# Performance work log

Hardware: AMD Instinct MI355X
Metric: run time of the kernel (lower is better)

## Reference

```python
import jax, jax.numpy as jnp
import numpy as np

B, T, D, H = 4, 2048, 1024, 16
HD = D // H  # head_dim = 64


def setup_inputs() -> dict:
    key = jax.random.key(0)
    k1, k2, k3 = jax.random.split(key, 3)
    x = jax.random.normal(k1, (B, T, D), dtype=jnp.float32)
    # Linear weights stored [in, out] (transpose of torch's [out, in]); scaled init.
    w_qkv = jax.random.normal(k2, (D, 3 * D), dtype=jnp.float32) / np.sqrt(D)
    b_qkv = jnp.zeros((3 * D,), dtype=jnp.float32)
    w_out = jax.random.normal(k3, (D, D), dtype=jnp.float32) / np.sqrt(D)
    b_out = jnp.zeros((D,), dtype=jnp.float32)
    # Causal mask [1,1,T,T]: 1 where attention allowed (j<=i), 0 elsewhere.
    causal_mask = jnp.tril(jnp.ones((T, T), dtype=jnp.int32))[None, None]
    return {"x": x, "causal_mask": causal_mask, "w_qkv": w_qkv,
            "b_qkv": b_qkv, "w_out": w_out, "b_out": b_out}


def reference(x, causal_mask, w_qkv, b_qkv, w_out, b_out):
    b, t, c = x.shape
    qkv = x @ w_qkv + b_qkv                         # [B,T,3D]
    qkv = qkv.reshape(b, t, 3, H, HD)
    q, k, v = jnp.moveaxis(qkv, 2, 0)               # each [B,T,H,HD]
    q = q.transpose(0, 2, 1, 3)                     # [B,H,T,HD]
    k = k.transpose(0, 2, 1, 3)
    v = v.transpose(0, 2, 1, 3)
    att = jnp.einsum('bhqd,bhkd->bhqk', q, k) / np.sqrt(HD).astype(np.float32)
    att = jnp.where(causal_mask == 0, jnp.float32(-jnp.inf), att)
    att = jax.nn.softmax(att, axis=-1)              # dropout=0.0 (eval)
    y = jnp.einsum('bhqk,bhkd->bhqd', att, v)       # [B,H,T,HD]
    y = y.transpose(0, 2, 1, 3).reshape(b, t, c)    # [B,T,D]
    return y @ w_out + b_out
```

## Files before the change

kernel.cpp:

```cpp
#include <hip/hip_runtime.h>
#include <hip/hip_bf16.h>
#include <stdint.h>

#define BB 4
#define TT 2048
#define DD 1024
#define HH 16
#define HDD 64
#define M1 (BB*TT)
#define N1 (3*DD)
#define KDIM DD

typedef __attribute__((ext_vector_type(8))) short short8;
typedef __attribute__((ext_vector_type(4))) float f32x4;

#if __has_builtin(__builtin_amdgcn_exp2f)
#define EXP2(x) __builtin_amdgcn_exp2f(x)
#else
#define EXP2(x) exp2f(x)
#endif

#define GLOAD_LDS16(gp, lp) \
    __builtin_amdgcn_global_load_lds( \
        (const __attribute__((address_space(1))) void*)(gp), \
        (__attribute__((address_space(3))) void*)(lp), 16, 0, 0)

__device__ __forceinline__ float bf2f(unsigned short u) {
    union { uint32_t u32; float f; } c; c.u32 = ((uint32_t)u) << 16; return c.f;
}
__device__ __forceinline__ unsigned short f2bf(float f) {
    union { float f; uint32_t u32; } c; c.f = f;
    uint32_t u = c.u32;
    return (unsigned short)((u + 0x7FFFu + ((u >> 16) & 1u)) >> 16);
}

template <int CTRL>
__device__ __forceinline__ float dpp_ror(float x) {
    union { float f; int i; } u, r;
    u.f = x;
    r.i = __builtin_amdgcn_update_dpp(u.i, u.i, CTRL, 0xF, 0xF, false);
    return r.f;
}
__device__ __forceinline__ float red_max16(float x) {
    x = fmaxf(x, dpp_ror<0x128>(x));
    x = fmaxf(x, dpp_ror<0x124>(x));
    x = fmaxf(x, dpp_ror<0x122>(x));
    x = fmaxf(x, dpp_ror<0x121>(x));
    return x;
}
__device__ __forceinline__ float red_sum16(float x) {
    x += dpp_ror<0x128>(x);
    x += dpp_ror<0x124>(x);
    x += dpp_ror<0x122>(x);
    x += dpp_ror<0x121>(x);
    return x;
}

__global__ __launch_bounds__(256) void cvt_f32_bf16(
    const float* __restrict__ in, unsigned short* __restrict__ out, int n4)
{
    int i = blockIdx.x * 256 + threadIdx.x;
    if (i >= n4) return;
    float4 v = *(const float4*)&in[(size_t)i * 4];
    ushort4 o;
    o.x = f2bf(v.x); o.y = f2bf(v.y); o.z = f2bf(v.z); o.w = f2bf(v.w);
    *(ushort4*)&out[(size_t)i * 4] = o;
}

__global__ __launch_bounds__(256) void transpose_f32_bf16(
    const float* __restrict__ in, unsigned short* __restrict__ out,
    int R, int C)
{
    __shared__ unsigned short tile[32][33];
    int bx = blockIdx.x;
    int by = blockIdx.y;
    int x = bx*32 + threadIdx.x;
    int y0 = by*32 + threadIdx.y;
    #pragma unroll
    for (int i = 0; i < 32; i += 8)
        tile[threadIdx.y + i][threadIdx.x] = f2bf(in[(size_t)(y0 + i)*C + x]);
    __syncthreads();
    int xo = by*32 + threadIdx.x;
    int yo = bx*32 + threadIdx.y;
    #pragma unroll
    for (int i = 0; i < 32; i += 8)
        out[(size_t)(yo + i)*R + xo] = tile[threadIdx.x][threadIdx.y + i];
}

template <int MODE, int BM, int BN>
__global__ __launch_bounds__(512, 2) void gemm_big(
    const unsigned short* __restrict__ A, const unsigned short* __restrict__ BT,
    const float* __restrict__ bias, void* __restrict__ Cout, void* __restrict__ Cout2,
    int K, int N, int NXT)
{
    constexpr int SHSZ = 2*(BM+BN)*64;
    __shared__ __align__(16) unsigned short Sh[SHSZ];

    const int tid  = threadIdx.x;
    const int lane = tid & 63;
    const int wave = tid >> 6;
    constexpr int WNG = BN/64;
    const int wm = wave / WNG, wn = wave % WNG;
    const int quad = lane >> 4, l16 = lane & 15;

    const int nwg = gridDim.x, cpx = nwg >> 3;
    const int wg = (blockIdx.x & 7)*cpx + (blockIdx.x >> 3);
    const int by = wg / NXT, bx = wg - by*NXT;
    const int m0 = by*BM, n0 = bx*BN;

    f32x4 acc[4][4] = {};
    const int nk = K >> 6;

    auto STAGE = [&](int t, int buf) {
        const int k0 = t << 6;
        unsigned short* Ab = &Sh[buf*(BM*64)];
        unsigned short* Bb = &Sh[2*BM*64 + buf*(BN*64)];
        #pragma unroll
        for (int p = 0; p < BM/64; ++p) {
            int c = p*512 + tid;
            int row = c >> 3, ch = (c & 7) ^ (row & 7);
            GLOAD_LDS16(&A[(size_t)(m0 + row)*K + k0 + ch*8], &Ab[c*8]);
        }
        #pragma unroll
        for (int p = 0; p < BN/64; ++p) {
            int c = p*512 + tid;
            int row = c >> 3, ch = (c & 7) ^ (row & 7);
            GLOAD_LDS16(&BT[(size_t)(n0 + row)*K + k0 + ch*8], &Bb[c*8]);
        }
    };

    STAGE(0, 0);
    STAGE(1, 1);

    for (int t = 0; t < nk; ++t) {
        const int buf = t & 1;
        const unsigned short* Ab = &Sh[buf*(BM*64)];
        const unsigned short* Bb = &Sh[2*BM*64 + buf*(BN*64)];

        if (t == nk - 1) asm volatile("s_waitcnt vmcnt(0)" ::: "memory");
        else             asm volatile("s_waitcnt vmcnt(6)" ::: "memory");
        __builtin_amdgcn_s_barrier();
        __builtin_amdgcn_sched_barrier(0);

        short8 fa[4][2], fb[2][2];

        #pragma unroll
        for (int mi = 0; mi < 4; ++mi)
            #pragma unroll
            for (int kk = 0; kk < 2; ++kk) {
                int row = wm*64 + mi*16 + l16;
                fa[mi][kk] = *(const short8*)&Ab[row*64 + (((kk*4 + quad) ^ (row & 7))*8)];
            }
        #pragma unroll
        for (int ni = 0; ni < 2; ++ni)
            #pragma unroll
            for (int kk = 0; kk < 2; ++kk) {
                int row = wn*64 + ni*16 + l16;
                fb[ni][kk] = *(const short8*)&Bb[row*64 + (((kk*4 + quad) ^ (row & 7))*8)];
            }
        __builtin_amdgcn_s_barrier();
        __builtin_amdgcn_s_setprio(1);
        #pragma unroll
        for (int mi = 0; mi < 4; ++mi)
            #pragma unroll
            for (int ni = 0; ni < 2; ++ni)
                #pragma unroll
                for (int kk = 0; kk < 2; ++kk)
                    acc[mi][ni] = __builtin_amdgcn_mfma_f32_16x16x32_bf16(
                        fa[mi][kk], fb[ni][kk], acc[mi][ni], 0, 0, 0);
        __builtin_amdgcn_s_setprio(0);
        __builtin_amdgcn_s_barrier();

        #pragma unroll
        for (int ni = 0; ni < 2; ++ni)
            #pragma unroll
            for (int kk = 0; kk < 2; ++kk) {
                int row = wn*64 + 32 + ni*16 + l16;
                fb[ni][kk] = *(const short8*)&Bb[row*64 + (((kk*4 + quad) ^ (row & 7))*8)];
            }
        __builtin_amdgcn_s_barrier();
        __builtin_amdgcn_s_setprio(1);
        #pragma unroll
        for (int mi = 0; mi < 4; ++mi)
            #pragma unroll
            for (int ni = 0; ni < 2; ++ni)
                #pragma unroll
                for (int kk = 0; kk < 2; ++kk)
                    acc[mi][2 + ni] = __builtin_amdgcn_mfma_f32_16x16x32_bf16(
                        fa[mi][kk], fb[ni][kk], acc[mi][2 + ni], 0, 0, 0);
        __builtin_amdgcn_s_setprio(0);
        __builtin_amdgcn_s_barrier();

        __builtin_amdgcn_sched_barrier(0);
        if (t + 2 < nk) STAGE(t + 2, buf);
    }

    if (MODE == 2 && n0 >= 2048) {
        constexpr int STR = BM + 8;
        #pragma unroll
        for (int ni = 0; ni < 4; ++ni) {
            int nl = wn*64 + ni*16 + l16;
            float bv = bias[n0 + nl];
            #pragma unroll
            for (int mi = 0; mi < 4; ++mi) {
                ushort4 pk;
                pk.x = f2bf(acc[mi][ni][0] + bv);
                pk.y = f2bf(acc[mi][ni][1] + bv);
                pk.z = f2bf(acc[mi][ni][2] + bv);
                pk.w = f2bf(acc[mi][ni][3] + bv);
                *(ushort4*)&Sh[nl*STR + wm*64 + mi*16 + quad*4] = pk;
            }
        }
        __builtin_amdgcn_s_barrier();
        const int bb = m0 >> 11, t0 = m0 & 2047;
        constexpr int CHROW = BM/8;
        constexpr int NIT = BN*CHROW/512;
        #pragma unroll
        for (int p = 0; p < NIT; ++p) {
            int c = p*512 + tid;
            int row = c / CHROW, ch = c % CHROW;
            int nv = n0 + row - 2048;
            int hv = nv >> 6, dv = nv & 63;
            *(uint4*)&((unsigned short*)Cout2)[((size_t)((bb*16 + hv)*64 + dv))*2048 + t0 + ch*8] =
                *(uint4*)&Sh[row*STR + ch*8];
        }
        return;
    }

    const int cstride = (MODE == 2) ? 2048 : N;
    #pragma unroll
    for (int ni = 0; ni < 4; ++ni) {
        int n = n0 + wn*64 + ni*16 + l16;
        float bv = bias[n];
        #pragma unroll
        for (int mi = 0; mi < 4; ++mi) {
            #pragma unroll
            for (int r = 0; r < 4; ++r) {
                int m = m0 + wm*64 + mi*16 + quad*4 + r;
                float val = acc[mi][ni][r] + bv;
                if (MODE == 1)
                    ((float*)Cout)[(size_t)m*cstride + n] = val;
                else
                    ((unsigned short*)Cout)[(size_t)m*cstride + n] = f2bf(val);
            }
        }
    }
}

#define PST 72
__global__ __launch_bounds__(256, 3) void attn_mfma(
    const unsigned short* __restrict__ QK, const unsigned short* __restrict__ VT,
    unsigned short* __restrict__ Y)
{
    __shared__ __align__(16) unsigned short Sh[16384 + 4*32*PST];

    const int tid  = threadIdx.x;
    const int lane = tid & 63;
    const int wave = tid >> 6;
    const int quad = lane >> 4, l16 = lane & 15;

    const int i = blockIdx.x;
    const int xcd = i & 7, j = i >> 3;
    const int a = j & 7;
    const int u = j >> 3;
    const int bh2 = xcd + 8*u;
    const int b = bh2 >> 4, h = bh2 & 15;
    const size_t qkbase = (size_t)(b*TT) * 2048;
    const size_t vbase  = (size_t)(bh2*64) * 2048;
    const int qcol = h*64, kcol = 1024 + h*64;
    const float C2 = 0.18033688011112042f;

    unsigned short* Pw = &Sh[16384 + wave*(32*PST)];

    const int nk1 = 2*a + 2;
    const int ntot = 34;

    short8 aq[2][2];
    f32x4 o[2][4];
    float mold[2][4], lsum[2][4];
    int q0w = a*128 + wave*32;

    auto LOADQ = [&]() {
        #pragma unroll
        for (int mt = 0; mt < 2; ++mt)
            #pragma unroll
            for (int kk = 0; kk < 2; ++kk)
                aq[mt][kk] = *(const short8*)&QK[qkbase + (size_t)(q0w + mt*16 + l16)*2048
                                                + qcol + kk*32 + quad*8];
        #pragma unroll
        for (int mt = 0; mt < 2; ++mt)
            #pragma unroll
            for (int r = 0; r < 4; ++r) { mold[mt][r] = -3.0e38f; lsum[mt][r] = 0.0f; }
        #pragma unroll
        for (int mt = 0; mt < 2; ++mt)
            #pragma unroll
            for (int dt = 0; dt < 4; ++dt) { f32x4 z = {}; o[mt][dt] = z; }
    };
    auto FINALIZE = [&]() {
        #pragma unroll
        for (int mt = 0; mt < 2; ++mt)
            #pragma unroll
            for (int r = 0; r < 4; ++r) {
                float inv = 1.0f / lsum[mt][r];
                int tq = q0w + mt*16 + quad*4 + r;
                #pragma unroll
                for (int dt = 0; dt < 4; ++dt)
                    Y[((size_t)(b*TT + tq))*DD + h*64 + dt*16 + l16] = f2bf(o[mt][dt][r] * inv);
            }
    };

    auto STAGE = [&](int buf, int k0) {
        unsigned short* Kb = &Sh[buf*4096];
        unsigned short* Vb = &Sh[8192 + buf*4096];
        #pragma unroll
        for (int p = 0; p < 2; ++p) {
            int c = p*256 + tid;
            int r = c >> 3;
            int ch = (c & 7) ^ (r & 7);
            GLOAD_LDS16(&QK[qkbase + (size_t)(k0 + r)*2048 + kcol + ch*8], &Kb[c*8]);
        }
        #pragma unroll
        for (int p = 0; p < 2; ++p) {
            int c = p*256 + tid;
            int r = c >> 3;
            int ch = (c & 7) ^ (r & 7);
            GLOAD_LDS16(&VT[vbase + (size_t)r*2048 + k0 + ch*8], &Vb[c*8]);
        }
    };

    LOADQ();
    STAGE(0, 0);
    asm volatile("s_waitcnt vmcnt(0)" ::: "memory");
    __builtin_amdgcn_s_barrier();

    int cur = 0;
    for (int t = 0; t < ntot; ++t) {
        const int k0 = ((t < nk1) ? t : t - nk1) * 64;
        if (t + 1 < ntot) {
            const int t1 = t + 1;
            STAGE(cur ^ 1, ((t1 < nk1) ? t1 : t1 - nk1) * 64);
        }
        if (t == nk1) {
            FINALIZE();
            q0w = (15 - a)*128 + wave*32;
            LOADQ();
        }

        if (k0 <= q0w + 31) {
            const unsigned short* Kb = &Sh[cur*4096];
            const unsigned short* Vb = &Sh[8192 + cur*4096];

            f32x4 s[2][4];
            #pragma unroll
            for (int nt = 0; nt < 4; ++nt) {
                if (k0 + nt*16 <= q0w + 31) {
                    f32x4 z = {};
                    s[0][nt] = z; s[1][nt] = z;
                    #pragma unroll
                    for (int kk = 0; kk < 2; ++kk) {
                        int r = nt*16 + l16;
                        short8 bk = *(const short8*)&Kb[r*64 + (((kk*4 + quad) ^ (r & 7))*8)];
                        s[0][nt] = __builtin_amdgcn_mfma_f32_16x16x32_bf16(aq[0][kk], bk, s[0][nt], 0, 0, 0);
                        s[1][nt] = __builtin_amdgcn_mfma_f32_16x16x32_bf16(aq[1][kk], bk, s[1][nt], 0, 0, 0);
                    }
                } else {
                    #pragma unroll
                    for (int r = 0; r < 4; ++r) { s[0][nt][r] = -3.0e38f; s[1][nt][r] = -3.0e38f; }
                }
            }

            short8 bv[2][4];
            #pragma unroll
            for (int kk = 0; kk < 2; ++kk)
                #pragma unroll
                for (int dt = 0; dt < 4; ++dt) {
                    int r = dt*16 + l16;
                    bv[kk][dt] = *(const short8*)&Vb[r*64 + (((kk*4 + quad) ^ (r & 7))*8)];
                }

            if (k0 + 63 > q0w) {
                #pragma unroll
                for (int mt = 0; mt < 2; ++mt)
                    #pragma unroll
                    for (int nt = 0; nt < 4; ++nt)
                        #pragma unroll
                        for (int r = 0; r < 4; ++r) {
                            int kg = k0 + nt*16 + l16;
                            int qg = q0w + mt*16 + quad*4 + r;
                            if (kg > qg) s[mt][nt][r] = -3.0e38f;
                        }
            }

            float m2n[2][4], al[2][4];
            #pragma unroll
            for (int mt = 0; mt < 2; ++mt)
                #pragma unroll
                for (int r = 0; r < 4; ++r) {
                    float rm = fmaxf(fmaxf(s[mt][0][r], s[mt][1][r]),
                                     fmaxf(s[mt][2][r], s[mt][3][r]));
                    rm = red_max16(rm);
                    float m2 = fmaxf(mold[mt][r], rm * C2);
                    al[mt][r]  = EXP2(mold[mt][r] - m2);
                    m2n[mt][r] = m2;
                }
            float rs[2][4] = {};
            #pragma unroll
            for (int mt = 0; mt < 2; ++mt)
                #pragma unroll
                for (int nt = 0; nt < 4; ++nt)
                    #pragma unroll
                    for (int r = 0; r < 4; ++r) {
                        float p = EXP2(fmaf(s[mt][nt][r], C2, -m2n[mt][r]));
                        s[mt][nt][r] = p;
                        rs[mt][r] += p;
                    }
            #pragma unroll
            for (int mt = 0; mt < 2; ++mt)
                #pragma unroll
                for (int r = 0; r < 4; ++r) {
                    float tsum = red_sum16(rs[mt][r]);
                    lsum[mt][r] = lsum[mt][r]*al[mt][r] + tsum;
                    mold[mt][r] = m2n[mt][r];
                }

            #pragma unroll
            for (int mt = 0; mt < 2; ++mt)
                #pragma unroll
                for (int nt = 0; nt < 4; ++nt)
                    #pragma unroll
                    for (int r = 0; r < 4; ++r) {
                        union { float f; uint32_t u; } c; c.f = s[mt][nt][r];
                        Pw[(mt*16 + quad*4 + r)*PST + nt*16 + l16] =
                            (unsigned short)((c.u + 0x8000u) >> 16);
                    }

            #pragma unroll
            for (int mt = 0; mt < 2; ++mt)
                #pragma unroll
                for (int dt = 0; dt < 4; ++dt)
                    #pragma unroll
                    for (int r = 0; r < 4; ++r)
                        o[mt][dt][r] *= al[mt][r];
            #pragma unroll
            for (int kk = 0; kk < 2; ++kk) {
                short8 ap0 = *(short8*)&Pw[(     l16)*PST + kk*32 + quad*8];
                short8 ap1 = *(short8*)&Pw[(16 + l16)*PST + kk*32 + quad*8];
                #pragma unroll
                for (int dt = 0; dt < 4; ++dt) {
                    o[0][dt] = __builtin_amdgcn_mfma_f32_16x16x32_bf16(ap0, bv[kk][dt], o[0][dt], 0, 0, 0);
                    o[1][dt] = __builtin_amdgcn_mfma_f32_16x16x32_bf16(ap1, bv[kk][dt], o[1][dt], 0, 0, 0);
                }
            }
        }

        asm volatile("s_waitcnt vmcnt(0)" ::: "memory");
        __builtin_amdgcn_s_barrier();
        cur ^= 1;
    }

    FINALIZE();
}

extern "C" void kernel_launch(void* const* d_in, const int* in_sizes, int n_in,
                              void* d_out, int out_size, void* d_ws, size_t ws_size,
                              hipStream_t stream)
{
    const float* x    = (const float*)d_in[0];
    const float* wqkv = (const float*)d_in[2];
    const float* bqkv = (const float*)d_in[3];
    const float* wout = (const float*)d_in[4];
    const float* bout = (const float*)d_in[5];
    float* out = (float*)d_out;

    char* ws = (char*)d_ws;
    unsigned short* Xb    = (unsigned short*)ws;
    unsigned short* WqkvT = (unsigned short*)(ws + 16777216);
    unsigned short* WoutT = (unsigned short*)(ws + 23068672);
    unsigned short* QK    = (unsigned short*)(ws + 25165824);
    unsigned short* VTb   = (unsigned short*)(ws + 58720256);
    unsigned short* Ybuf  = (unsigned short*)(ws + 75497472);

    cvt_f32_bf16<<<(M1*KDIM/4 + 255)/256, 256, 0, stream>>>(x, Xb, M1*KDIM/4);
    transpose_f32_bf16<<<dim3(N1/32, KDIM/32), dim3(32, 8), 0, stream>>>(wqkv, WqkvT, KDIM, N1);
    transpose_f32_bf16<<<dim3(DD/32, KDIM/32), dim3(32, 8), 0, stream>>>(wout, WoutT, KDIM, DD);
    gemm_big<2, 256, 128><<<dim3(768), 512, 0, stream>>>(Xb, WqkvT, bqkv, QK, VTb, KDIM, N1, 24);
    attn_mfma<<<dim3(512), 256, 0, stream>>>(QK, VTb, Ybuf);
    gemm_big<1, 128, 256><<<dim3(256), 512, 0, stream>>>(Ybuf, WoutT, bout, out, nullptr, KDIM, DD, 4);
}
```

Before: 313.7 us.

## Triple-buffer GEMM LDS and interleave prefetch loads across four MFMA phases

The GEMM main loop moves from two LDS buffers to three rotating buffers. The global-to-LDS prefetch for tile t+2 is split into six parts that are issued between four MFMA sub-phases, instead of in one burst at the end of each iteration. Fragment loads are also regrouped into quadrants so fewer registers are live at once. The aim is to overlap memory traffic with compute and shorten stalls at the loop tail, at the cost of 1.5x the LDS footprint, which may reduce occupancy, and extra barriers per iteration. The vmcnt(6) wait count may no longer match the new per-phase load pattern.

```diff
diff --git a/kernel.cpp b/kernel.cpp
--- a/kernel.cpp
+++ b/kernel.cpp
@@ -93,13 +93,14 @@
     const float* __restrict__ bias, void* __restrict__ Cout, void* __restrict__ Cout2,
     int K, int N, int NXT)
 {
-    constexpr int SHSZ = 2*(BM+BN)*64;
-    __shared__ __align__(16) unsigned short Sh[SHSZ];
+    constexpr int TBUF = (BM + BN) * 64;
+    constexpr int NPART = (BM + BN) / 64;
+    __shared__ __align__(16) unsigned short Sh[3 * TBUF];
 
     const int tid  = threadIdx.x;
     const int lane = tid & 63;
     const int wave = tid >> 6;
-    constexpr int WNG = BN/64;
+    constexpr int WNG = BN / 64;
     const int wm = wave / WNG, wn = wave % WNG;
     const int quad = lane >> 4, l16 = lane & 15;
 
@@ -111,88 +112,124 @@
     f32x4 acc[4][4] = {};
     const int nk = K >> 6;
 
-    auto STAGE = [&](int t, int buf) {
-        const int k0 = t << 6;
-        unsigned short* Ab = &Sh[buf*(BM*64)];
-        unsigned short* Bb = &Sh[2*BM*64 + buf*(BN*64)];
-        #pragma unroll
-        for (int p = 0; p < BM/64; ++p) {
-            int c = p*512 + tid;
+    auto STAGE_PART = [&](int tt, int bufi, int part) {
+        const int k0 = tt << 6;
+        unsigned short* base = &Sh[bufi * TBUF];
+        if ((part + 1) * 512 <= BM * 8) {
+            int c = part*512 + tid;
             int row = c >> 3, ch = (c & 7) ^ (row & 7);
-            GLOAD_LDS16(&A[(size_t)(m0 + row)*K + k0 + ch*8], &Ab[c*8]);
-        }
-        #pragma unroll
-        for (int p = 0; p < BN/64; ++p) {
-            int c = p*512 + tid;
+            GLOAD_LDS16(&A[(size_t)(m0 + row)*K + k0 + ch*8], &base[c*8]);
+        } else {
+            int c = part*512 + tid - BM*8;
             int row = c >> 3, ch = (c & 7) ^ (row & 7);
-            GLOAD_LDS16(&BT[(size_t)(n0 + row)*K + k0 + ch*8], &Bb[c*8]);
+            GLOAD_LDS16(&BT[(size_t)(n0 + row)*K + k0 + ch*8], &base[BM*64 + c*8]);
         }
     };
 
-    STAGE(0, 0);
-    STAGE(1, 1);
-
+    #pragma unroll
+    for (int p = 0; p < NPART; ++p) STAGE_PART(0, 0, p);
+    #pragma unroll
+    for (int p = 0; p < NPART; ++p) STAGE_PART(1, 1, p);
+
+    int bR = 0;
     for (int t = 0; t < nk; ++t) {
-        const int buf = t & 1;
-        const unsigned short* Ab = &Sh[buf*(BM*64)];
-        const unsigned short* Bb = &Sh[2*BM*64 + buf*(BN*64)];
-
-        if (t == nk - 1) asm volatile("s_waitcnt vmcnt(0)" ::: "memory");
+        const unsigned short* Ab = &Sh[bR * TBUF];
+        const unsigned short* Bb = &Sh[bR * TBUF + BM*64];
+        const int bS = (bR + 2 >= 3) ? bR - 1 : bR + 2;
+        const bool pf = (t + 2 < nk);
+
+        if (t >= nk - 1) asm volatile("s_waitcnt vmcnt(0)" ::: "memory");
         else             asm volatile("s_waitcnt vmcnt(6)" ::: "memory");
         __builtin_amdgcn_s_barrier();
         __builtin_amdgcn_sched_barrier(0);
 
-        short8 fa[4][2], fb[2][2];
-
-        #pragma unroll
-        for (int mi = 0; mi < 4; ++mi)
+        short8 fa0[2][2], fa1[2][2], fb0[2][2], fb1[2][2];
+
+        #pragma unroll
+        for (int i = 0; i < 2; ++i)
             #pragma unroll
             for (int kk = 0; kk < 2; ++kk) {
-                int row = wm*64 + mi*16 + l16;
-                fa[mi][kk] = *(const short8*)&Ab[row*64 + (((kk*4 + quad) ^ (row & 7))*8)];
-            }
-        #pragma unroll
-        for (int ni = 0; ni < 2; ++ni)
+                int row = wm*64 + i*16 + l16;
+                fa0[i][kk] = *(const short8*)&Ab[row*64 + (((kk*4 + quad) ^ (row & 7))*8)];
+            }
+        #pragma unroll
+        for (int j = 0; j < 2; ++j)
             #pragma unroll
             for (int kk = 0; kk < 2; ++kk) {
-                int row = wn*64 + ni*16 + l16;
-                fb[ni][kk] = *(const short8*)&Bb[row*64 + (((kk*4 + quad) ^ (row & 7))*8)];
-            }
+                int row = wn*64 + j*16 + l16;
+                fb0[j][kk] = *(const short8*)&Bb[row*64 + (((kk*4 + quad) ^ (row & 7))*8)];
+            }
+        if (pf) { STAGE_PART(t+2, bS, 0); STAGE_PART(t+2, bS, 1); }
         __builtin_amdgcn_s_barrier();
         __builtin_amdgcn_s_setprio(1);
         #pragma unroll
-        for (int mi = 0; mi < 4; ++mi)
-            #pragma unroll
-            for (int ni = 0; ni < 2; ++ni)
+        for (int i = 0; i < 2; ++i)
+            #pragma unroll
+            for (int j = 0; j < 2; ++j)
                 #pragma unroll
                 for (int kk = 0; kk < 2; ++kk)
-                    acc[mi][ni] = __builtin_amdgcn_mfma_f32_16x16x32_bf16(
-                        fa[mi][kk], fb[ni][kk], acc[mi][ni], 0, 0, 0);
+                    acc[i][j] = __builtin_amdgcn_mfma_f32_16x16x32_bf16(
+                        fa0[i][kk], fb0[j][kk], acc[i][j], 0, 0, 0);
         __builtin_amdgcn_s_setprio(0);
         __builtin_amdgcn_s_barrier();
 
         #pragma unroll
-        for (int ni = 0; ni < 2; ++ni)
+        for (int j = 0; j < 2; ++j)
             #pragma unroll
             for (int kk = 0; kk < 2; ++kk) {
-                int row = wn*64 + 32 + ni*16 + l16;
-                fb[ni][kk] = *(const short8*)&Bb[row*64 + (((kk*4 + quad) ^ (row & 7))*8)];
-            }
+                int row = wn*64 + 32 + j*16 + l16;
+                fb1[j][kk] = *(const short8*)&Bb[row*64 + (((kk*4 + quad) ^ (row & 7))*8)];
+            }
+        if (pf) { STAGE_PART(t+2, bS, 2); STAGE_PART(t+2, bS, 3); }
         __builtin_amdgcn_s_barrier();
         __builtin_amdgcn_s_setprio(1);
         #pragma unroll
-        for (int mi = 0; mi < 4; ++mi)
-            #pragma unroll
-            for (int ni = 0; ni < 2; ++ni)
+        for (int i = 0; i < 2; ++i)
+            #pragma unroll
+            for (int j = 0; j < 2; ++j)
                 #pragma unroll
                 for (int kk = 0; kk < 2; ++kk)
-                    acc[mi][2 + ni] = __builtin_amdgcn_mfma_f32_16x16x32_bf16(
-                        fa[mi][kk], fb[ni][kk], acc[mi][2 + ni], 0, 0, 0);
+                    acc[i][2+j] = __builtin_amdgcn_mfma_f32_16x16x32_bf16(
+                        fa0[i][kk], fb1[j][kk], acc[i][2+j], 0, 0, 0);
         __builtin_amdgcn_s_setprio(0);
         __builtin_amdgcn_s_barrier();
 
-        __builtin_amdgcn_sched_barrier(0);
-        if (t + 2 < nk) STAGE(t + 2, buf);
+        #pragma unroll
+        for (int i = 0; i < 2; ++i)
+            #pragma unroll
+            for (int kk = 0; kk < 2; ++kk) {
+                int row = wm*64 + 32 + i*16 + l16;
+                fa1[i][kk] = *(const short8*)&Ab[row*64 + (((kk*4 + quad) ^ (row & 7))*8)];
+            }
+        if (pf) STAGE_PART(t+2, bS, 4);
+        __builtin_amdgcn_s_barrier();
+        __builtin_amdgcn_s_setprio(1);
+        #pragma unroll
+        for (int i = 0; i < 2; ++i)
+            #pragma unroll
+            for (int j = 0; j < 2; ++j)
+                #pragma unroll
+                for (int kk = 0; kk < 2; ++kk)
+                    acc[2+i][2+j] = __builtin_amdgcn_mfma_f32_16x16x32_bf16(
+                        fa1[i][kk], fb1[j][kk], acc[2+i][2+j], 0, 0, 0);
+        __builtin_amdgcn_s_setprio(0);
+        __builtin_amdgcn_s_barrier();
+
+        if (pf) STAGE_PART(t+2, bS, 5);
+        __builtin_amdgcn_s_barrier();
+        __builtin_amdgcn_s_setprio(1);
+        #pragma unroll
+        for (int i = 0; i < 2; ++i)
+            #pragma unroll
+            for (int j = 0; j < 2; ++j)
+                #pragma unroll
+                for (int kk = 0; kk < 2; ++kk)
+                    acc[2+i][j] = __builtin_amdgcn_mfma_f32_16x16x32_bf16(
+                        fa1[i][kk], fb0[j][kk], acc[2+i][j], 0, 0, 0);
+        __builtin_amdgcn_s_setprio(0);
+        __builtin_amdgcn_s_barrier();
+
+        bR = (bR + 1 >= 3) ? 0 : bR + 1;
     }
 
     if (MODE == 2 && n0 >= 2048) {
```

Measured after the change: 323.8 us. 1.03x slower.

## Add 256x256 eight-phase pipelined GEMM for the QKV projection

Applied to the files above, without the earlier changes.

Adds a new GEMM kernel with 256x256 tiles that splits each 64-wide K step into half-tile stages. Loads for later K steps are interleaved with MFMA phases under explicit waitcnt and barrier control. The QKV projection now runs on this kernel, using 384 workgroups instead of 768 with 128x256 tiles. The larger tile raises operand reuse per byte loaded and hides global-to-LDS latency, at the cost of more accumulator registers, 128 KB of LDS, and fewer workgroups, which lowers occupancy and worsens tail balance.

```diff
diff --git a/kernel.cpp b/kernel.cpp
--- a/kernel.cpp
+++ b/kernel.cpp
@@ -87,6 +87,257 @@
         out[(size_t)(yo + i)*R + xo] = tile[threadIdx.x][threadIdx.y + i];
 }
 
+#define GTSTR 264
+template <int MODE>
+__global__ __launch_bounds__(512, 2) void gemm8p(
+    const unsigned short* __restrict__ A, const unsigned short* __restrict__ BT,
+    const float* __restrict__ bias, void* __restrict__ Cout, void* __restrict__ Cout2,
+    int K, int N, int NXT)
+{
+    constexpr int SHSZ = (MODE == 2) ? 256*GTSTR : 65536;
+    __shared__ __align__(16) unsigned short Sh[SHSZ];
+
+    const int tid  = threadIdx.x;
+    const int lane = tid & 63;
+    const int wave = tid >> 6;
+    const int wm = wave >> 2, wn = wave & 3;
+    const int quad = lane >> 4, l16 = lane & 15;
+
+    const int nwg = gridDim.x, cpx = nwg >> 3;
+    const int wg = (blockIdx.x & 7)*cpx + (blockIdx.x >> 3);
+    const int by = wg / NXT, bx = wg - by*NXT;
+    const int m0 = by*256, n0 = bx*256;
+
+    f32x4 acc[8][4] = {};
+    const int nk = K >> 6;
+
+    auto SA = [&](int d, int h) -> unsigned short* { return &Sh[(d*2 + h)*16384]; };
+    auto SB = [&](int d, int h) -> unsigned short* { return &Sh[(d*2 + h)*16384 + 8192]; };
+
+    auto STG_A = [&](int d, int h, int t) {
+        const int k0 = t << 6;
+        unsigned short* dst = SA(d, h);
+        #pragma unroll
+        for (int p = 0; p < 2; ++p) {
+            int c = p*512 + tid;
+            int rl = c >> 3, ch = (c & 7) ^ (rl & 7);
+            GLOAD_LDS16(&A[(size_t)(m0 + h*128 + rl)*K + k0 + ch*8], &dst[c*8]);
+        }
+    };
+    auto STG_B = [&](int d, int h, int t) {
+        const int k0 = t << 6;
+        unsigned short* dst = SB(d, h);
+        #pragma unroll
+        for (int p = 0; p < 2; ++p) {
+            int c = p*512 + tid;
+            int rl = c >> 3, ch = (c & 7) ^ (rl & 7);
+            GLOAD_LDS16(&BT[(size_t)(n0 + h*128 + rl)*K + k0 + ch*8], &dst[c*8]);
+        }
+    };
+    auto RA = [&](int d, int mf, int kk) -> short8 {
+        int rl = mf*16 + l16;
+        return *(const short8*)&SA(d, wm)[rl*64 + (((kk*4 + quad) ^ (rl & 7))*8)];
+    };
+    auto RB = [&](int d, int nf, int kk) -> short8 {
+        int rl = (wn & 1)*64 + nf*16 + l16;
+        return *(const short8*)&SB(d, wn >> 1)[rl*64 + (((kk*4 + quad) ^ (rl & 7))*8)];
+    };
+
+    STG_A(0, 0, 0); STG_A(0, 1, 0); STG_B(0, 0, 0); STG_B(0, 1, 0);
+    STG_A(1, 0, 1);
+    asm volatile("s_waitcnt vmcnt(2)" ::: "memory");
+    __builtin_amdgcn_s_barrier();
+    __builtin_amdgcn_sched_barrier(0);
+
+    for (int i = 0; i < nk/2; ++i) {
+        const int tb = 2*i + 1, tn0 = 2*i + 2, tn1 = 2*i + 3;
+        const bool p2 = (tn0 < nk), p3 = (tn1 < nk);
+        short8 a0[4][2], a1[4][2], b0[2][2], b1[2][2];
+
+        #pragma unroll
+        for (int mf = 0; mf < 4; ++mf) { a0[mf][0] = RA(0, mf, 0); a0[mf][1] = RA(0, mf, 1); }
+        #pragma unroll
+        for (int nf = 0; nf < 2; ++nf) { b0[nf][0] = RB(0, nf, 0); b0[nf][1] = RB(0, nf, 1); }
+        STG_A(1, 1, tb);
+        __builtin_amdgcn_s_barrier();
+        __builtin_amdgcn_s_setprio(1);
+        #pragma unroll
+        for (int mf = 0; mf < 4; ++mf)
+            #pragma unroll
+            for (int nf = 0; nf < 2; ++nf)
+                #pragma unroll
+                for (int kk = 0; kk < 2; ++kk)
+                    acc[mf][nf] = __builtin_amdgcn_mfma_f32_16x16x32_bf16(
+                        a0[mf][kk], b0[nf][kk], acc[mf][nf], 0, 0, 0);
+        __builtin_amdgcn_s_setprio(0);
+        __builtin_amdgcn_s_barrier();
+
+        #pragma unroll
+        for (int nf = 0; nf < 2; ++nf) { b1[nf][0] = RB(0, 2+nf, 0); b1[nf][1] = RB(0, 2+nf, 1); }
+        STG_B(1, 0, tb);
+        __builtin_amdgcn_s_barrier();
+        __builtin_amdgcn_s_setprio(1);
+        #pragma unroll
+        for (int mf = 0; mf < 4; ++mf)
+            #pragma unroll
+            for (int nf = 0; nf < 2; ++nf)
+                #pragma unroll
+                for (int kk = 0; kk < 2; ++kk)
+                    acc[mf][2+nf] = __builtin_amdgcn_mfma_f32_16x16x32_bf16(
+                        a0[mf][kk], b1[nf][kk], acc[mf][2+nf], 0, 0, 0);
+        __builtin_amdgcn_s_setprio(0);
+        __builtin_amdgcn_s_barrier();
+
+        #pragma unroll
+        for (int mf = 0; mf < 4; ++mf) { a1[mf][0] = RA(0, 4+mf, 0); a1[mf][1] = RA(0, 4+mf, 1); }
+        STG_B(1, 1, tb);
+        __builtin_amdgcn_s_barrier();
+        __builtin_amdgcn_s_setprio(1);
+        #pragma unroll
+        for (int mf = 0; mf < 4; ++mf)
+            #pragma unroll
+            for (int nf = 0; nf < 2; ++nf)
+                #pragma unroll
+                for (int kk = 0; kk < 2; ++kk)
+                    acc[4+mf][nf] = __builtin_amdgcn_mfma_f32_16x16x32_bf16(
+                        a1[mf][kk], b0[nf][kk], acc[4+mf][nf], 0, 0, 0);
+        __builtin_amdgcn_s_setprio(0);
+        __builtin_amdgcn_s_barrier();
+
+        if (p2) STG_A(0, 0, tn0);
+        __builtin_amdgcn_s_barrier();
+        __builtin_amdgcn_s_setprio(1);
+        #pragma unroll
+        for (int mf = 0; mf < 4; ++mf)
+            #pragma unroll
+            for (int nf = 0; nf < 2; ++nf)
+                #pragma unroll
+                for (int kk = 0; kk < 2; ++kk)
+                    acc[4+mf][2+nf] = __builtin_amdgcn_mfma_f32_16x16x32_bf16(
+                        a1[mf][kk], b1[nf][kk], acc[4+mf][2+nf], 0, 0, 0);
+        __builtin_amdgcn_s_setprio(0);
+        if (p2) asm volatile("s_waitcnt vmcnt(2)" ::: "memory");
+        else    asm volatile("s_waitcnt vmcnt(0)" ::: "memory");
+        __builtin_amdgcn_s_barrier();
+        __builtin_amdgcn_sched_barrier(0);
+
+        #pragma unroll
+        for (int mf = 0; mf < 4; ++mf) { a0[mf][0] = RA(1, mf, 0); a0[mf][1] = RA(1, mf, 1); }
+        #pragma unroll
+        for (int nf = 0; nf < 2; ++nf) { b0[nf][0] = RB(1, nf, 0); b0[nf][1] = RB(1, nf, 1); }
+        if (p2) STG_A(0, 1, tn0);
+        __builtin_amdgcn_s_barrier();
+        __builtin_amdgcn_s_setprio(1);
+        #pragma unroll
+        for (int mf = 0; mf < 4; ++mf)
+            #pragma unroll
+            for (int nf = 0; nf < 2; ++nf)
+                #pragma unroll
+                for (int kk = 0; kk < 2; ++kk)
+                    acc[mf][nf] = __builtin_amdgcn_mfma_f32_16x16x32_bf16(
+                        a0[mf][kk], b0[nf][kk], acc[mf][nf], 0, 0, 0);
+        __builtin_amdgcn_s_setprio(0);
+        __builtin_amdgcn_s_barrier();
+
+        #pragma unroll
+        for (int nf = 0; nf < 2; ++nf) { b1[nf][0] = RB(1, 2+nf, 0); b1[nf][1] = RB(1, 2+nf, 1); }
+        if (p2) STG_B(0, 0, tn0);
+        __builtin_amdgcn_s_barrier();
+        __builtin_amdgcn_s_setprio(1);
+        #pragma unroll
+        for (int mf = 0; mf < 4; ++mf)
+            #pragma unroll
+            for (int nf = 0; nf < 2; ++nf)
+                #pragma unroll
+                for (int kk = 0; kk < 2; ++kk)
+                    acc[mf][2+nf] = __builtin_amdgcn_mfma_f32_16x16x32_bf16(
+                        a0[mf][kk], b1[nf][kk], acc[mf][2+nf], 0, 0, 0);
+        __builtin_amdgcn_s_setprio(0);
+        __builtin_amdgcn_s_barrier();
+
+        #pragma unroll
+        for (int mf = 0; mf < 4; ++mf) { a1[mf][0] = RA(1, 4+mf, 0); a1[mf][1] = RA(1, 4+mf, 1); }
+        if (p2) STG_B(0, 1, tn0);
+        __builtin_amdgcn_s_barrier();
+        __builtin_amdgcn_s_setprio(1);
+        #pragma unroll
+        for (int mf = 0; mf < 4; ++mf)
+            #pragma unroll
+            for (int nf = 0; nf < 2; ++nf)
+                #pragma unroll
+                for (int kk = 0; kk < 2; ++kk)
+                    acc[4+mf][nf] = __builtin_amdgcn_mfma_f32_16x16x32_bf16(
+                        a1[mf][kk], b0[nf][kk], acc[4+mf][nf], 0, 0, 0);
+        __builtin_amdgcn_s_setprio(0);
+        __builtin_amdgcn_s_barrier();
+
+        if (p3) STG_A(1, 0, tn1);
+        __builtin_amdgcn_s_barrier();
+        __builtin_amdgcn_s_setprio(1);
+        #pragma unroll
+        for (int mf = 0; mf < 4; ++mf)
+            #pragma unroll
+            for (int nf = 0; nf < 2; ++nf)
+                #pragma unroll
+                for (int kk = 0; kk < 2; ++kk)
+                    acc[4+mf][2+nf] = __builtin_amdgcn_mfma_f32_16x16x32_bf16(
+                        a1[mf][kk], b1[nf][kk], acc[4+mf][2+nf], 0, 0, 0);
+        __builtin_amdgcn_s_setprio(0);
+        if (p3) asm volatile("s_waitcnt vmcnt(2)" ::: "memory");
+        else    asm volatile("s_waitcnt vmcnt(0)" ::: "memory");
+        __builtin_amdgcn_s_barrier();
+        __builtin_amdgcn_sched_barrier(0);
+    }
+
+    if (MODE == 2 && n0 >= 2048) {
+        #pragma unroll
+        for (int ni = 0; ni < 4; ++ni) {
+            int nl = wn*64 + ni*16 + l16;
+            float bv = bias[n0 + nl];
+            #pragma unroll
+            for (int mi = 0; mi < 8; ++mi) {
+                ushort4 pk;
+                pk.x = f2bf(acc[mi][ni][0] + bv);
+                pk.y = f2bf(acc[mi][ni][1] + bv);
+                pk.z = f2bf(acc[mi][ni][2] + bv);
+                pk.w = f2bf(acc[mi][ni][3] + bv);
+                *(ushort4*)&Sh[nl*GTSTR + wm*128 + mi*16 + quad*4] = pk;
+            }
+        }
+        __builtin_amdgcn_s_barrier();
+        const int bb = m0 >> 11, t0 = m0 & 2047;
+        #pragma unroll
+        for (int p = 0; p < 16; ++p) {
+            int c = p*512 + tid;
+            int row = c >> 5, ch = c & 31;
+            int nv = n0 + row - 2048;
+            int hv = nv >> 6, dv = nv & 63;
+            *(uint4*)&((unsigned short*)Cout2)[((size_t)((bb*16 + hv)*64 + dv))*2048 + t0 + ch*8] =
+                *(uint4*)&Sh[row*GTSTR + ch*8];
+        }
+        return;
+    }
+
+    const int cstride = (MODE == 2) ? 2048 : N;
+    #pragma unroll
+    for (int ni = 0; ni < 4; ++ni) {
+        int n = n0 + wn*64 + ni*16 + l16;
+        float bv = bias[n];
+        #pragma unroll
+        for (int mi = 0; mi < 8; ++mi) {
+            #pragma unroll
+            for (int r = 0; r < 4; ++r) {
+                int m = m0 + wm*128 + mi*16 + quad*4 + r;
+                float val = acc[mi][ni][r] + bv;
+                if (MODE == 1)
+                    ((float*)Cout)[(size_t)m*cstride + n] = val;
+                else
+                    ((unsigned short*)Cout)[(size_t)m*cstride + n] = f2bf(val);
+            }
+        }
+    }
+}
+
 template <int MODE, int BM, int BN>
 __global__ __launch_bounds__(512, 2) void gemm_big(
     const unsigned short* __restrict__ A, const unsigned short* __restrict__ BT,
@@ -193,38 +444,6 @@
 
         __builtin_amdgcn_sched_barrier(0);
         if (t + 2 < nk) STAGE(t + 2, buf);
-    }
-
-    if (MODE == 2 && n0 >= 2048) {
-        constexpr int STR = BM + 8;
-        #pragma unroll
-        for (int ni = 0; ni < 4; ++ni) {
-            int nl = wn*64 + ni*16 + l16;
-            float bv = bias[n0 + nl];
-            #pragma unroll
-            for (int mi = 0; mi < 4; ++mi) {
-                ushort4 pk;
-                pk.x = f2bf(acc[mi][ni][0] + bv);
-                pk.y = f2bf(acc[mi][ni][1] + bv);
-                pk.z = f2bf(acc[mi][ni][2] + bv);
-                pk.w = f2bf(acc[mi][ni][3] + bv);
-                *(ushort4*)&Sh[nl*STR + wm*64 + mi*16 + quad*4] = pk;
-            }
-        }
-        __builtin_amdgcn_s_barrier();
-        const int bb = m0 >> 11, t0 = m0 & 2047;
-        constexpr int CHROW = BM/8;
-        constexpr int NIT = BN*CHROW/512;
-        #pragma unroll
-        for (int p = 0; p < NIT; ++p) {
-            int c = p*512 + tid;
-            int row = c / CHROW, ch = c % CHROW;
-            int nv = n0 + row - 2048;
-            int hv = nv >> 6, dv = nv & 63;
-            *(uint4*)&((unsigned short*)Cout2)[((size_t)((bb*16 + hv)*64 + dv))*2048 + t0 + ch*8] =
-                *(uint4*)&Sh[row*STR + ch*8];
-        }
-        return;
     }
 
     const int cstride = (MODE == 2) ? 2048 : N;
@@ -483,7 +702,7 @@
     cvt_f32_bf16<<<(M1*KDIM/4 + 255)/256, 256, 0, stream>>>(x, Xb, M1*KDIM/4);
     transpose_f32_bf16<<<dim3(N1/32, KDIM/32), dim3(32, 8), 0, stream>>>(wqkv, WqkvT, KDIM, N1);
     transpose_f32_bf16<<<dim3(DD/32, KDIM/32), dim3(32, 8), 0, stream>>>(wout, WoutT, KDIM, DD);
-    gemm_big<2, 256, 128><<<dim3(768), 512, 0, stream>>>(Xb, WqkvT, bqkv, QK, VTb, KDIM, N1, 24);
+    gemm8p<2><<<dim3(384), 512, 0, stream>>>(Xb, WqkvT, bqkv, QK, VTb, KDIM, N1, 12);
     attn_mfma<<<dim3(512), 256, 0, stream>>>(QK, VTb, Ybuf);
     gemm_big<1, 128, 256><<<dim3(256), 512, 0, stream>>>(Ybuf, WoutT, bout, out, nullptr, KDIM, DD, 4);
 }
```

Measured after the change: 312.3 us. About the same (-0.4%).
